# Kernel optimization log

Hardware: AMD Instinct MI355X
Metric: run time of the kernel (lower is better)

Reference implementation:

```python
import jax, jax.numpy as jnp
import numpy as np

PROPOSAL_COUNT = 100
IOU_THRESHOLD = 0.3
SCORE_THRESHOLD = 0.7
MEAN = np.array([0.0, 0.0, 0.0, 0.0], np.float32)
STD = np.array([0.1, 0.1, 0.2, 0.2], np.float32)
CLIP_RATIO = 16.0 / 1000.0
NEG = -1e9  # finite -inf sentinel (avoids NaNs)


def delta2bbox(anchors, delta):
    # anchors: (..., 4) xyxy, delta: (..., 4) normalized dx,dy,dw,dh
    delta = delta * STD + MEAN
    w = anchors[..., 2] - anchors[..., 0]
    h = anchors[..., 3] - anchors[..., 1]
    cx = anchors[..., 0] + 0.5 * w
    cy = anchors[..., 1] + 0.5 * h
    max_ratio = abs(float(np.log(CLIP_RATIO)))
    dx, dy = delta[..., 0], delta[..., 1]
    dw = jnp.clip(delta[..., 2], -max_ratio, max_ratio)
    dh = jnp.clip(delta[..., 3], -max_ratio, max_ratio)
    pcx = cx + dx * w
    pcy = cy + dy * h
    pw = w * jnp.exp(dw)
    ph = h * jnp.exp(dh)
    return jnp.stack([pcx - 0.5 * pw, pcy - 0.5 * ph, pcx + 0.5 * pw, pcy + 0.5 * ph], axis=-1)


def iou_one(box, boxes):
    # box: (4,), boxes: (N, 4) -> (N,)
    ix1 = jnp.maximum(box[0], boxes[..., 0])
    iy1 = jnp.maximum(box[1], boxes[..., 1])
    ix2 = jnp.minimum(box[2], boxes[..., 2])
    iy2 = jnp.minimum(box[3], boxes[..., 3])
    inter = jnp.maximum(ix2 - ix1, 0.0) * jnp.maximum(iy2 - iy1, 0.0)
    area1 = (box[2] - box[0]) * (box[3] - box[1])
    area2 = (boxes[..., 2] - boxes[..., 0]) * (boxes[..., 3] - boxes[..., 1])
    return inter / jnp.maximum(area1 + area2 - inter, 1e-9)


def greedy_nms(scores, boxes):
    # masked greedy hard-NMS with fixed PROPOSAL_COUNT iterations
    # scores: (N,) with NEG on invalid entries, boxes: (N, 4)
    def step(s, _):
        i = jnp.argmax(s)
        si = s[i]
        sel = si > 0.5 * NEG
        iou = iou_one(boxes[i], boxes)
        s = jnp.where(sel & (iou > IOU_THRESHOLD), NEG, s)
        s = s.at[i].set(NEG)
        return s, (jnp.where(sel, i, -1), jnp.where(sel, si, NEG))
    _, (idx, sc) = jax.lax.scan(step, scores, None, length=PROPOSAL_COUNT)
    return idx, sc  # (P,), (P,)


def filter_detection(logits, regress, anchors):
    B, N, C = logits.shape
    # decode + clip (elementwise, same math as gathering first then decoding)
    boxes = jnp.clip(delta2bbox(anchors[None], regress), 0.0, 1.0)  # (B,N,4)
    label = jnp.argmax(logits, axis=-1)                             # (B,N)
    fg = label > 0                                                  # background filter
    scores = jnp.moveaxis(logits[..., 1:], -1, 1)                   # (B,C-1,N)
    valid = fg[:, None, :] & (scores >= SCORE_THRESHOLD)
    s0 = jnp.where(valid, scores, NEG)
    # selection indices are piecewise constant in the inputs
    s0_c = jax.lax.stop_gradient(s0)
    boxes_c = jax.lax.stop_gradient(boxes)
    nms_b = jax.vmap(jax.vmap(greedy_nms, in_axes=(0, None)), in_axes=(0, 0))
    sel_idx, sel_sc = nms_b(s0_c, boxes_c)                          # (B,C-1,P)
    K = (C - 1) * PROPOSAL_COUNT
    idx_flat = sel_idx.reshape(B, K)
    sc_flat = sel_sc.reshape(B, K)
    # global top-k over all classes, sorted descending (matches tf.nn.top_k)
    top_sc, top_pos = jax.lax.top_k(sc_flat, PROPOSAL_COUNT)        # (B,P)
    anchor_idx = jnp.take_along_axis(idx_flat, top_pos, axis=1)
    ok = (top_sc > 0.5 * NEG)[..., None].astype(logits.dtype)       # padding mask
    safe = jnp.maximum(anchor_idx, 0)
    out_logit = jnp.take_along_axis(logits, safe[..., None], axis=1) * ok  # (B,P,C)
    out_box = jnp.take_along_axis(boxes, safe[..., None], axis=1) * ok     # (B,P,4)
    return out_logit, out_box


def setup_inputs() -> dict:
    key = jax.random.key(0)
    k1, k2, k3, k4 = jax.random.split(key, 4)
    B, N, C = 4, 100000, 41
    logits = jax.random.normal(k1, (B, N, C), jnp.float32)
    regress = jax.random.normal(k2, (B, N, 4), jnp.float32) * 0.5
    xy = jax.random.uniform(k3, (N, 2), jnp.float32) * 0.8
    wh = jax.random.uniform(k4, (N, 2), jnp.float32) * 0.2 + 0.01
    anchors = jnp.concatenate([xy, jnp.minimum(xy + wh, 1.0)], axis=-1)  # valid xyxy in [0,1]
    return {"logits": logits, "regress": regress, "anchors": anchors}


def reference(logits, regress, anchors):
    return filter_detection(logits, regress, anchors)
```

## Files before the change

kernel.cpp:

```cpp
#include <hip/hip_runtime.h>
#include <cstdint>
#include <cstddef>

#define BN 4
#define NN 100000
#define CC 41
#define NCLS 40
#define NPROB (BN * NCLS)
#define PROP 100
#define NEGV (-1e9f)
#define IOU_T 0.3f
#define SCORE_T 0.7f
#define MAXR 4.135166556742356f
#define CAP 2048
#define TARGET 384
#define LISTCAP 26624
#define NBMPW 3125
#define E07 0xBF333333u
#define ERHI 0xC1800000u
#define W0 ((unsigned long long)(ERHI - E07))
#define NT3 512
#define CHK 8192
#define NCHKB 4

typedef unsigned long long ull;
typedef unsigned int uint;

__device__ __forceinline__ uint encf(float x) {
  uint u = __float_as_uint(x);
  return (u & 0x80000000u) ? ~u : (u | 0x80000000u);
}
__device__ __forceinline__ float decf(uint e) {
  uint u = (e & 0x80000000u) ? (e ^ 0x80000000u) : ~e;
  return __uint_as_float(u);
}
__device__ __forceinline__ uint binofE(ull E) {
  return (E >= (ull)ERHI) ? 255u : (uint)(((E - E07) << 8) / W0);
}
__device__ __forceinline__ ull edgeE(int b) {
  return (ull)E07 + (((ull)b * W0 + 255ull) >> 8);
}

__device__ __forceinline__ float iou_f(float ax1, float ay1, float ax2, float ay2,
                                       float bx1, float by1, float bx2, float by2) {
  float ix1 = fmaxf(ax1, bx1), iy1 = fmaxf(ay1, by1);
  float ix2 = fminf(ax2, bx2), iy2 = fminf(ay2, by2);
  float inter = fmaxf(ix2 - ix1, 0.0f) * fmaxf(iy2 - iy1, 0.0f);
  float a1 = (ax2 - ax1) * (ay2 - ay1);
  float a2 = (bx2 - bx1) * (by2 - by1);
  return inter / fmaxf(a1 + a2 - inter, 1e-9f);
}

__device__ __forceinline__ int select_window(const uint* h, int* lo_out) {
  uint cum = 0; int lo = 256; int act = 2;
  for (int bb = 255; bb >= 0; --bb) {
    uint nb = h[bb];
    if (nb == 0u) continue;
    if (cum + nb > CAP) {
      if (cum == 0u) { act = 1; }
      break;
    }
    cum += nb; lo = bb; act = 0;
    if (cum >= TARGET) break;
  }
  *lo_out = lo;
  return act;
}

__global__ void decode_kernel(const float4* __restrict__ regress,
                              const float4* __restrict__ anchors,
                              float4* __restrict__ boxes,
                              uint* __restrict__ gcnt) {
  int i = blockIdx.x * 256 + threadIdx.x;
  if (i < NPROB) gcnt[i] = 0u;
  if (i >= BN * NN) return;
  int n = i % NN;
  float4 d = regress[i];
  float4 a = anchors[n];
  float w = a.z - a.x, h = a.w - a.y;
  float cx = a.x + 0.5f * w, cy = a.y + 0.5f * h;
  float dx = d.x * 0.1f, dy = d.y * 0.1f;
  float dw = fminf(fmaxf(d.z * 0.2f, -MAXR), MAXR);
  float dh = fminf(fmaxf(d.w * 0.2f, -MAXR), MAXR);
  float pcx = cx + dx * w, pcy = cy + dy * h;
  float pw = w * expf(dw), ph = h * expf(dh);
  float4 o;
  o.x = fminf(fmaxf(pcx - 0.5f * pw, 0.0f), 1.0f);
  o.y = fminf(fmaxf(pcy - 0.5f * ph, 0.0f), 1.0f);
  o.z = fminf(fmaxf(pcx + 0.5f * pw, 0.0f), 1.0f);
  o.w = fminf(fmaxf(pcy + 0.5f * ph, 0.0f), 1.0f);
  boxes[i] = o;
}

__global__ void score_kernel(const float* __restrict__ logits,
                             ull* __restrict__ glist,
                             uint* __restrict__ gcnt,
                             uint* __restrict__ fgb) {
  __shared__ float lg[256 * CC];
  __shared__ unsigned short wpre[NCLS][4];
  __shared__ uint cbase[NCLS];
  int b = blockIdx.y;
  int n0 = blockIdx.x * 256;
  int tid = threadIdx.x;
  int wave = tid >> 6, lane = tid & 63;
  int rows = NN - n0; if (rows > 256) rows = 256;
  int total4 = rows * CC / 4;
  const float4* src = (const float4*)(logits + ((size_t)b * NN + n0) * CC);
  float4* dst = (float4*)lg;
  for (int i = tid; i < total4; i += 256) dst[i] = src[i];
  __syncthreads();

  bool act = tid < rows;
  int n = n0 + tid;
  float bestv = 0.0f; int bestc = 0;
  if (act) {
    bestv = lg[tid * CC];
    #pragma unroll
    for (int c = 1; c < CC; ++c) {
      float v = lg[tid * CC + c];
      if (v > bestv) { bestv = v; bestc = c; }
    }
  }
  bool fg = act && (bestc > 0);
  int wbase = n0 + (tid & ~63);

  ull mfg = __ballot(fg);
  if (lane == 0 && wbase < NN) fgb[b * NBMPW + (wbase >> 5)] = (uint)mfg;
  if (lane == 32 && wbase + 32 < NN) fgb[b * NBMPW + (wbase >> 5) + 1] = (uint)(mfg >> 32);

  #pragma unroll 4
  for (int c = 1; c < CC; ++c) {
    float v = act ? lg[tid * CC + c] : 0.0f;
    ull m = __ballot(fg && (v >= SCORE_T));
    if (lane == 0) wpre[c - 1][wave] = (unsigned short)__popcll(m);
  }
  __syncthreads();

  if (tid < NCLS) {
    uint t0 = wpre[tid][0], t1 = wpre[tid][1], t2 = wpre[tid][2], t3 = wpre[tid][3];
    uint tot = t0 + t1 + t2 + t3;
    uint base = tot ? atomicAdd(&gcnt[b * NCLS + tid], tot) : 0u;
    cbase[tid] = base;
    wpre[tid][0] = 0;
    wpre[tid][1] = (unsigned short)t0;
    wpre[tid][2] = (unsigned short)(t0 + t1);
    wpre[tid][3] = (unsigned short)(t0 + t1 + t2);
  }
  __syncthreads();

  #pragma unroll 4
  for (int c = 1; c < CC; ++c) {
    float v = act ? lg[tid * CC + c] : 0.0f;
    bool elig = fg && (v >= SCORE_T);
    ull m = __ballot(elig);
    if (elig) {
      uint pos = cbase[c - 1] + wpre[c - 1][wave]
               + (uint)__popcll(m & ((1ull << lane) - 1ull));
      if (pos < LISTCAP)
        glist[(size_t)(b * NCLS + (c - 1)) * LISTCAP + pos] =
            ((ull)encf(v) << 32) | (uint)n;
    }
  }
}

__global__ void hist_kernel(const ull* __restrict__ glist,
                            const uint* __restrict__ gcnt,
                            uint* __restrict__ chist) {
  __shared__ uint h[256];
  int prob = blockIdx.y;
  int chunk = blockIdx.x;
  int tid = threadIdx.x;
  uint cnt = gcnt[prob];
  h[tid] = 0u;
  __syncthreads();
  if (cnt <= LISTCAP) {
    uint lo = chunk * CHK;
    uint hi = cnt < lo + CHK ? cnt : lo + CHK;
    const ull* list = glist + (size_t)prob * LISTCAP;
    for (uint i = lo + tid; i < hi; i += 256)
      atomicAdd(&h[binofE(list[i] >> 32)], 1u);
  }
  __syncthreads();
  chist[((size_t)prob * NCHKB + chunk) * 256 + tid] = h[tid];
}

__global__ void offsets_kernel(const uint* __restrict__ chist,
                               const uint* __restrict__ gcnt,
                               uint* __restrict__ gcoff,
                               uint* __restrict__ gC) {
  __shared__ uint sa[256], sb[256];
  int prob = blockIdx.x;
  int tid = threadIdx.x;
  uint cnt = gcnt[prob];
  if (cnt > LISTCAP) return;
  const uint* ch = chist + (size_t)prob * NCHKB * 256;
  uint h0 = ch[0 * 256 + tid], h1 = ch[1 * 256 + tid],
       h2 = ch[2 * 256 + tid], h3 = ch[3 * 256 + tid];
  gcoff[((size_t)prob * NCHKB + 0) * 256 + tid] = 0u;
  gcoff[((size_t)prob * NCHKB + 1) * 256 + tid] = h0;
  gcoff[((size_t)prob * NCHKB + 2) * 256 + tid] = h0 + h1;
  gcoff[((size_t)prob * NCHKB + 3) * 256 + tid] = h0 + h1 + h2;
  sa[tid] = h0 + h1 + h2 + h3;
  __syncthreads();
  uint* s = sa; uint* d = sb;
  for (int off = 1; off < 256; off <<= 1) {
    uint v = s[tid] + ((tid + off < 256) ? s[tid + off] : 0u);
    d[tid] = v;
    __syncthreads();
    uint* t = s; s = d; d = t;
  }
  gC[(size_t)prob * 257 + tid] = s[tid];
  if (tid == 0) gC[(size_t)prob * 257 + 256] = 0u;
}

__global__ void scatter_kernel(const ull* __restrict__ glist,
                               const uint* __restrict__ gcnt,
                               const uint* __restrict__ gcoff,
                               const uint* __restrict__ gC,
                               ull* __restrict__ blist) {
  __shared__ uint rank[256], startL[256], cofL[256];
  int prob = blockIdx.y;
  int chunk = blockIdx.x;
  int tid = threadIdx.x;
  uint cnt = gcnt[prob];
  if (cnt > LISTCAP) return;
  rank[tid] = 0u;
  cofL[tid] = gcoff[((size_t)prob * NCHKB + chunk) * 256 + tid];
  startL[tid] = gC[(size_t)prob * 257 + tid + 1];
  __syncthreads();
  uint lo = chunk * CHK;
  uint hi = cnt < lo + CHK ? cnt : lo + CHK;
  const ull* list = glist + (size_t)prob * LISTCAP;
  ull* bl = blist + (size_t)prob * LISTCAP;
  for (uint i = lo + tid; i < hi; i += 256) {
    ull k = list[i];
    uint bin = binofE(k >> 32);
    uint r = atomicAdd(&rank[bin], 1u);
    bl[startL[bin] + cofL[bin] + r] = k;
  }
}

__device__ int sort_walk(int ncand, int nsel,
                         ull* keysL, float4* boxesL, float4* selL,
                         int* sh_nsel, int prob, int* __restrict__ oidx,
                         float* __restrict__ osc, int tid) {
  if (ncand == 0) return nsel;
  int M = 64; while (M < ncand) M <<= 1;
  for (int i = ncand + tid; i < M; i += NT3) keysL[i] = 0ull;
  __syncthreads();
  for (int k = 2; k <= M; k <<= 1) {
    for (int j = k >> 1; j > 0; j >>= 1) {
      for (int t = tid; t < M; t += NT3) {
        int ixj = t ^ j;
        if (ixj > t) {
          ull a = keysL[t], c2 = keysL[ixj];
          bool up = ((t & k) == 0);
          if (up ? (a < c2) : (a > c2)) { keysL[t] = c2; keysL[ixj] = a; }
        }
      }
      __syncthreads();
    }
  }
  if (tid < 64) {
    int lane = tid;
    int ns = nsel;
    for (int base = 0; base < ncand && ns < PROP; base += 64) {
      int i = base + lane;
      bool valid = i < ncand;
      ull key = valid ? keysL[i] : 0ull;
      int slot = (int)(key & 0x7FFF);
      float4 bx = boxesL[valid ? slot : 0];
      float sc = decf((uint)(key >> 32));
      int aidx = 131071 - (int)((key >> 15) & 0x1FFFF);
      bool supp = false;
      for (int j = 0; j < ns; ++j) {
        float4 sb = selL[j];
        supp = supp || (iou_f(bx.x, bx.y, bx.z, bx.w, sb.x, sb.y, sb.z, sb.w) > IOU_T);
      }
      ull live = __ballot(valid && !supp);
      while (live && ns < PROP) {
        int kk = __ffsll(live) - 1;
        float x1 = __shfl(bx.x, kk), y1 = __shfl(bx.y, kk);
        float x2 = __shfl(bx.z, kk), y2 = __shfl(bx.w, kk);
        float ksc = __shfl(sc, kk);
        int kidx = __shfl(aidx, kk);
        if (lane == 0) {
          oidx[prob * PROP + ns] = kidx;
          osc [prob * PROP + ns] = ksc;
          selL[ns] = make_float4(x1, y1, x2, y2);
        }
        ns++;
        if (lane > kk && valid && !supp)
          supp = iou_f(bx.x, bx.y, bx.z, bx.w, x1, y1, x2, y2) > IOU_T;
        live = __ballot(valid && !supp) & ~((2ull << kk) - 1ull);
      }
    }
    if (lane == 0) *sh_nsel = ns;
  }
  __syncthreads();
  return *sh_nsel;
}

__device__ int process_window(ull WLO, ull WUP, int idxbin,
                              bool dense, uint rs, uint re,
                              const ull* list, const float* lcol,
                              const uint* fgp, const float4* bx4,
                              ull* keysL, float4* boxesL, float4* selL,
                              int* sh_cnt, int* sh_nsel,
                              int nsel, int prob, int* __restrict__ oidx,
                              float* __restrict__ osc, int tid) {
  __syncthreads();
  if (tid == 0) *sh_cnt = 0;
  __syncthreads();
  if (!dense) {
    for (uint i = rs + tid; i < re; i += NT3) {
      ull k = list[i];
      ull E = k >> 32;
      uint idx = (uint)(k & 0xFFFFFFFFu);
      if (E >= WLO && E < WUP && (idxbin < 0 || (int)(idx >> 9) == idxbin)) {
        int slot = atomicAdd(sh_cnt, 1);
        if (slot < CAP) {
          keysL[slot] = (E << 32)
                      | ((ull)((131071u - idx) & 0x1FFFFu) << 15)
                      | (ull)slot;
          boxesL[slot] = bx4[idx];
        }
      }
    }
  } else {
    for (int i = tid; i < NN; i += NT3) {
      if (!((fgp[i >> 5] >> (i & 31)) & 1u)) continue;
      float s = lcol[(size_t)i * CC];
      if (s < SCORE_T) continue;
      ull E = encf(s);
      if (E >= WLO && E < WUP && (idxbin < 0 || (i >> 9) == idxbin)) {
        int slot = atomicAdd(sh_cnt, 1);
        if (slot < CAP) {
          keysL[slot] = (E << 32)
                      | ((ull)((131071u - (uint)i) & 0x1FFFFu) << 15)
                      | (ull)slot;
          boxesL[slot] = bx4[i];
        }
      }
    }
  }
  __syncthreads();
  int ncand = *sh_cnt; if (ncand > CAP) ncand = CAP;
  return sort_walk(ncand, nsel, keysL, boxesL, selL, sh_nsel, prob, oidx, osc, tid);
}

__device__ int fallback_range(ull Rlo0, ull Rhi0,
                              bool dense, uint rs, uint re,
                              const ull* list, const float* lcol,
                              const uint* fgp, const float4* bx4,
                              ull* keysL, float4* boxesL, float4* selL,
                              uint* subh,
                              int* sh_cnt, int* sh_nsel, int* sh_a, int* sh_b,
                              int nsel, int prob, int* __restrict__ oidx,
                              float* __restrict__ osc, int tid) {
  ull EHIl = Rhi0;
  for (int round = 0; round < 300 && nsel < PROP; ++round) {
    ull Rlo = Rlo0, Rhi = EHIl;
    int action; int bsel;
    ull WLO = 0, WUP = 0, E0 = 0;
    bool idxm = false;
    while (true) {
      for (int i = tid; i < 256; i += NT3) subh[i] = 0u;
      __syncthreads();
      ull W = Rhi - Rlo;
      if (!dense) {
        for (uint i = rs + tid; i < re; i += NT3) {
          ull E = list[i] >> 32;
          if (E >= Rlo && E < Rhi)
            atomicAdd(&subh[(uint)(((E - Rlo) << 8) / W)], 1u);
        }
      } else {
        for (int i = tid; i < NN; i += NT3) {
          if (!((fgp[i >> 5] >> (i & 31)) & 1u)) continue;
          float s = lcol[(size_t)i * CC];
          if (s < SCORE_T) continue;
          ull E = encf(s);
          if (E >= Rlo && E < Rhi)
            atomicAdd(&subh[(uint)(((E - Rlo) << 8) / W)], 1u);
        }
      }
      __syncthreads();
      if (tid == 0) {
        int lo;
        int act = select_window(subh, &lo);
        int rb = -1;
        if (act == 1) {
          for (int bb = 255; bb >= 0; --bb) if (subh[bb]) { rb = bb; break; }
        }
        *sh_a = act; *sh_b = (act == 1) ? rb : lo;
      }
      __syncthreads();
      action = *sh_a; bsel = *sh_b;
      __syncthreads();
      if (action == 2) break;
      if (action == 0) {
        WLO = Rlo + (((ull)bsel * W + 255ull) >> 8);
        WUP = Rhi;
        break;
      }
      ull nRlo = Rlo + (((ull)bsel * W + 255ull) >> 8);
      ull nRhi = Rlo + (((ull)(bsel + 1) * W + 255ull) >> 8);
      if (nRhi > Rhi) nRhi = Rhi;
      Rlo = nRlo; Rhi = nRhi;
      if (Rhi - Rlo <= 1ull) { idxm = true; E0 = Rlo; break; }
    }
    if (action == 2) break;
    if (!idxm) {
      nsel = process_window(WLO, WUP, -1, dense, rs, re, list, lcol, fgp, bx4,
                            keysL, boxesL, selL, sh_cnt, sh_nsel,
                            nsel, prob, oidx, osc, tid);
      EHIl = WLO;
    } else {
      for (int ib = 0; ib < 256 && nsel < PROP; ++ib)
        nsel = process_window(E0, E0 + 1ull, ib, dense, rs, re, list, lcol, fgp, bx4,
                              keysL, boxesL, selL, sh_cnt, sh_nsel,
                              nsel, prob, oidx, osc, tid);
      EHIl = E0;
    }
  }
  return nsel;
}

__launch_bounds__(NT3)
__global__ void nms_finish(const ull* __restrict__ blist,
                           const uint* __restrict__ gcnt,
                           const float* __restrict__ logits,
                           const uint* __restrict__ fgb,
                           const float4* __restrict__ boxes,
                           const uint* __restrict__ gC,
                           int* __restrict__ oidx, float* __restrict__ osc) {
  __shared__ uint CL[257];
  __shared__ uint subh[256];
  __shared__ ull keysL[CAP];
  __shared__ float4 boxesL[CAP];
  __shared__ float4 selL[PROP];
  __shared__ int sh_cnt, sh_nsel, sh_a, sh_b, sh_m;

  int prob = blockIdx.x;
  int b = prob / NCLS;
  int c1 = prob % NCLS + 1;
  int tid = threadIdx.x;

  uint cnt = gcnt[prob];
  bool dense = cnt > LISTCAP;
  const ull* bl = blist + (size_t)prob * LISTCAP;
  const float4* bx4 = boxes + (size_t)b * NN;
  const float* lcol = logits + (size_t)b * NN * CC + c1;
  const uint* fgp = fgb + b * NBMPW;

  int nsel = 0;

  if (dense) {
    nsel = fallback_range(E07, 1ull << 32, true, 0, 0, bl, lcol, fgp, bx4,
                          keysL, boxesL, selL, subh, &sh_cnt, &sh_nsel, &sh_a, &sh_b,
                          0, prob, oidx, osc, tid);
  } else {
    for (int i = tid; i < 257; i += NT3) CL[i] = gC[(size_t)prob * 257 + i];
    __syncthreads();
    int hibin = 256;
    while (nsel < PROP && hibin > 0) {
      if (tid == 0) sh_m = -1;
      __syncthreads();
      if (tid < 256 && tid < hibin && (CL[tid] - CL[hibin]) >= TARGET)
        atomicMax(&sh_m, tid);
      __syncthreads();
      if (tid == 0) {
        int bm = sh_m; int act, lo;
        if (bm < 0) {
          uint W = CL[0] - CL[hibin];
          act = W ? 0 : 2; lo = 0;
        } else {
          uint W = CL[bm] - CL[hibin];
          if (W <= CAP) { act = 0; lo = bm; }
          else {
            uint W2 = CL[bm + 1] - CL[hibin];
            if (W2) { act = 0; lo = bm + 1; }
            else { act = 1; lo = bm; }
          }
        }
        sh_a = act; sh_b = lo;
      }
      __syncthreads();
      int act = sh_a, lo = sh_b;
      __syncthreads();
      if (act == 2) break;
      if (act == 0) {
        uint rs = CL[hibin];
        int ncand = (int)(CL[lo] - CL[hibin]);
        for (int i = tid; i < ncand; i += NT3) {
          ull k = bl[rs + i];
          uint idx = (uint)(k & 0xFFFFFFFFu);
          keysL[i] = ((k >> 32) << 32)
                   | ((ull)((131071u - idx) & 0x1FFFFu) << 15)
                   | (ull)i;
          boxesL[i] = bx4[idx];
        }
        __syncthreads();
        nsel = sort_walk(ncand, nsel, keysL, boxesL, selL, &sh_nsel, prob, oidx, osc, tid);
        hibin = lo;
      } else {
        uint rs = CL[lo + 1], re = CL[lo];
        ull Rlo = edgeE(lo);
        ull Rhi = (lo == 255) ? (1ull << 32) : edgeE(lo + 1);
        nsel = fallback_range(Rlo, Rhi, false, rs, re, bl, lcol, fgp, bx4,
                              keysL, boxesL, selL, subh, &sh_cnt, &sh_nsel, &sh_a, &sh_b,
                              nsel, prob, oidx, osc, tid);
        hibin = lo;
      }
    }
  }

  __syncthreads();
  for (int p = nsel + tid; p < PROP; p += NT3) {
    oidx[prob * PROP + p] = -1;
    osc [prob * PROP + p] = NEGV;
  }
}

__global__ void topk_kernel(const float* __restrict__ logits,
                            const float4* __restrict__ boxes,
                            const int* __restrict__ oidx,
                            const float* __restrict__ osc,
                            float* __restrict__ out) {
  __shared__ ull keys[4096];
  int b = blockIdx.x;
  int tid = threadIdx.x;
  for (int i = tid; i < 4096; i += 1024) {
    ull key = 0ull;
    if (i < NCLS * PROP) {
      float sc = osc[b * NCLS * PROP + i];
      key = ((ull)encf(sc) << 32) | (uint)(~i);
    }
    keys[i] = ~key;
  }
  __syncthreads();
  for (int k = 2; k <= 4096; k <<= 1) {
    for (int j = k >> 1; j > 0; j >>= 1) {
      for (int t = tid; t < 4096; t += 1024) {
        int ixj = t ^ j;
        if (ixj > t) {
          ull a = keys[t], c2 = keys[ixj];
          bool up = ((t & k) == 0);
          if ((a > c2) == up) { keys[t] = c2; keys[ixj] = a; }
        }
      }
      __syncthreads();
    }
  }
  if (tid < PROP) {
    ull key = ~keys[tid];
    uint e = (uint)(key >> 32);
    float sc = decf(e);
    bool ok = sc > 0.5f * NEGV;
    int kk = (int)(~(uint)key);
    if (kk < 0 || kk >= NCLS * PROP) kk = 0;
    int idx = ok ? oidx[b * NCLS * PROP + kk] : 0;
    if (idx < 0) idx = 0;
    float m = ok ? 1.0f : 0.0f;
    const float* lp = logits + ((size_t)b * NN + idx) * CC;
    float* outl = out + ((size_t)b * PROP + tid) * CC;
    #pragma unroll
    for (int c = 0; c < CC; ++c) outl[c] = lp[c] * m;
    float4 bb = boxes[(size_t)b * NN + idx];
    float* outb = out + (size_t)BN * PROP * CC + ((size_t)b * PROP + tid) * 4;
    outb[0] = bb.x * m; outb[1] = bb.y * m; outb[2] = bb.z * m; outb[3] = bb.w * m;
  }
}

extern "C" void kernel_launch(void* const* d_in, const int* in_sizes, int n_in,
                              void* d_out, int out_size, void* d_ws, size_t ws_size,
                              hipStream_t stream) {
  const float* logits  = (const float*)d_in[0];
  const float* regress = (const float*)d_in[1];
  const float* anchors = (const float*)d_in[2];
  float* out = (float*)d_out;

  char* ws = (char*)d_ws;
  size_t off = 0;
  float4* boxes = (float4*)(ws + off);  off += (size_t)BN * NN * 16;
  ull* glist = (ull*)(ws + off);        off += (size_t)NPROB * LISTCAP * 8;
  ull* blist = (ull*)(ws + off);        off += (size_t)NPROB * LISTCAP * 8;
  uint* gcnt = (uint*)(ws + off);       off += NPROB * 4;
  uint* fgb  = (uint*)(ws + off);       off += BN * NBMPW * 4;
  float* osc = (float*)(ws + off);      off += NPROB * PROP * 4;
  int*   oidx = (int*)(ws + off);       off += NPROB * PROP * 4;
  uint* chist = (uint*)(ws + off);      off += (size_t)NPROB * NCHKB * 256 * 4;
  uint* gcoff = (uint*)(ws + off);      off += (size_t)NPROB * NCHKB * 256 * 4;
  uint* gC   = (uint*)(ws + off);       off += (size_t)NPROB * 257 * 4;

  decode_kernel<<<(BN * NN + 255) / 256, 256, 0, stream>>>(
      (const float4*)regress, (const float4*)anchors, boxes, gcnt);
  score_kernel<<<dim3((NN + 255) / 256, BN), 256, 0, stream>>>(logits, glist, gcnt, fgb);
  hist_kernel<<<dim3(NCHKB, NPROB), 256, 0, stream>>>(glist, gcnt, chist);
  offsets_kernel<<<NPROB, 256, 0, stream>>>(chist, gcnt, gcoff, gC);
  scatter_kernel<<<dim3(NCHKB, NPROB), 256, 0, stream>>>(glist, gcnt, gcoff, gC, blist);
  nms_finish<<<NPROB, NT3, 0, stream>>>(blist, gcnt, logits, fgb, boxes, gC, oidx, osc);
  topk_kernel<<<BN, 1024, 0, stream>>>(logits, boxes, oidx, osc, out);
}
```

Before: 220.0 us.

## Shrink score kernel to single-wave blocks and drop LDS prefix sums

The score kernel now runs one 64-lane wave per block instead of four, so per-class counts come straight from ballots without shared-memory prefix arrays or extra block barriers. Each lane caches its logit row in registers, and the foreground test becomes a max over classes 1..40 compared with class 0. Lane c-1 issues the atomicAdd for class c and the base is broadcast with shuffles. The trade-off is four times as many blocks and four times as many global atomics, plus higher register pressure from holding 41 floats per lane.

```diff
diff --git a/kernel.cpp b/kernel.cpp
--- a/kernel.cpp
+++ b/kernel.cpp
@@ -92,70 +92,56 @@
   boxes[i] = o;
 }
 
-__global__ void score_kernel(const float* __restrict__ logits,
-                             ull* __restrict__ glist,
-                             uint* __restrict__ gcnt,
-                             uint* __restrict__ fgb) {
-  __shared__ float lg[256 * CC];
-  __shared__ unsigned short wpre[NCLS][4];
-  __shared__ uint cbase[NCLS];
+__global__ void __launch_bounds__(64)
+score_kernel(const float* __restrict__ logits,
+             ull* __restrict__ glist,
+             uint* __restrict__ gcnt,
+             uint* __restrict__ fgb) {
+  __shared__ float lg[64 * CC];
   int b = blockIdx.y;
-  int n0 = blockIdx.x * 256;
-  int tid = threadIdx.x;
-  int wave = tid >> 6, lane = tid & 63;
-  int rows = NN - n0; if (rows > 256) rows = 256;
+  int n0 = blockIdx.x * 64;
+  int lane = threadIdx.x;
+  int rows = NN - n0; if (rows > 64) rows = 64;
   int total4 = rows * CC / 4;
   const float4* src = (const float4*)(logits + ((size_t)b * NN + n0) * CC);
   float4* dst = (float4*)lg;
-  for (int i = tid; i < total4; i += 256) dst[i] = src[i];
-  __syncthreads();
-
-  bool act = tid < rows;
-  int n = n0 + tid;
-  float bestv = 0.0f; int bestc = 0;
-  if (act) {
-    bestv = lg[tid * CC];
-    #pragma unroll
-    for (int c = 1; c < CC; ++c) {
-      float v = lg[tid * CC + c];
-      if (v > bestv) { bestv = v; bestc = c; }
-    }
-  }
-  bool fg = act && (bestc > 0);
-  int wbase = n0 + (tid & ~63);
+  for (int i = lane; i < total4; i += 64) dst[i] = src[i];
+  __syncthreads();
+
+  bool act = lane < rows;
+  int n = n0 + lane;
+
+  float row[CC];
+  #pragma unroll
+  for (int c = 0; c < CC; ++c) row[c] = act ? lg[lane * CC + c] : 0.0f;
+
+  float m1 = row[1];
+  #pragma unroll
+  for (int c = 2; c < CC; ++c) m1 = fmaxf(m1, row[c]);
+  bool fg = act && (m1 > row[0]);
 
   ull mfg = __ballot(fg);
-  if (lane == 0 && wbase < NN) fgb[b * NBMPW + (wbase >> 5)] = (uint)mfg;
-  if (lane == 32 && wbase + 32 < NN) fgb[b * NBMPW + (wbase >> 5) + 1] = (uint)(mfg >> 32);
-
-  #pragma unroll 4
+  if (lane == 0) fgb[b * NBMPW + (n0 >> 5)] = (uint)mfg;
+  if (lane == 32 && n0 + 32 < NN) fgb[b * NBMPW + (n0 >> 5) + 1] = (uint)(mfg >> 32);
+
+  ull mym = 0ull;
+  #pragma unroll
   for (int c = 1; c < CC; ++c) {
-    float v = act ? lg[tid * CC + c] : 0.0f;
-    ull m = __ballot(fg && (v >= SCORE_T));
-    if (lane == 0) wpre[c - 1][wave] = (unsigned short)__popcll(m);
-  }
-  __syncthreads();
-
-  if (tid < NCLS) {
-    uint t0 = wpre[tid][0], t1 = wpre[tid][1], t2 = wpre[tid][2], t3 = wpre[tid][3];
-    uint tot = t0 + t1 + t2 + t3;
-    uint base = tot ? atomicAdd(&gcnt[b * NCLS + tid], tot) : 0u;
-    cbase[tid] = base;
-    wpre[tid][0] = 0;
-    wpre[tid][1] = (unsigned short)t0;
-    wpre[tid][2] = (unsigned short)(t0 + t1);
-    wpre[tid][3] = (unsigned short)(t0 + t1 + t2);
-  }
-  __syncthreads();
-
-  #pragma unroll 4
+    ull m = __ballot(fg && (row[c] >= SCORE_T));
+    if (lane == c - 1) mym = m;
+  }
+  uint base = 0u;
+  if (lane < NCLS && mym)
+    base = atomicAdd(&gcnt[b * NCLS + lane], (uint)__popcll(mym));
+
+  #pragma unroll
   for (int c = 1; c < CC; ++c) {
-    float v = act ? lg[tid * CC + c] : 0.0f;
+    float v = row[c];
     bool elig = fg && (v >= SCORE_T);
     ull m = __ballot(elig);
+    uint bc = __shfl(base, c - 1);
     if (elig) {
-      uint pos = cbase[c - 1] + wpre[c - 1][wave]
-               + (uint)__popcll(m & ((1ull << lane) - 1ull));
+      uint pos = bc + (uint)__popcll(m & ((1ull << lane) - 1ull));
       if (pos < LISTCAP)
         glist[(size_t)(b * NCLS + (c - 1)) * LISTCAP + pos] =
             ((ull)encf(v) << 32) | (uint)n;
@@ -595,7 +581,7 @@
 
   decode_kernel<<<(BN * NN + 255) / 256, 256, 0, stream>>>(
       (const float4*)regress, (const float4*)anchors, boxes, gcnt);
-  score_kernel<<<dim3((NN + 255) / 256, BN), 256, 0, stream>>>(logits, glist, gcnt, fgb);
+  score_kernel<<<dim3((NN + 63) / 64, BN), 64, 0, stream>>>(logits, glist, gcnt, fgb);
   hist_kernel<<<dim3(NCHKB, NPROB), 256, 0, stream>>>(glist, gcnt, chist);
   offsets_kernel<<<NPROB, 256, 0, stream>>>(chist, gcnt, gcoff, gC);
   scatter_kernel<<<dim3(NCHKB, NPROB), 256, 0, stream>>>(glist, gcnt, gcoff, gC, blist);
```

After: 260.4 us. 1.18x slower.

## Replace single-wave NMS walk with block-parallel bitmask suppression and larger windows

Applied to the files above, without the earlier changes.

Splits the sort+walk into a bitonic sort followed by a new walk that keeps a live-candidate bitmask in shared memory. Each selected box suppresses later candidates using all 512 threads rather than one wave. Candidate windows grow (TARGET 384→3072, CAP 2048→4096), so fewer window rounds run per class. The trade-off is one block-wide barrier per selected box, longer bitonic sorts over bigger windows, and more shared memory per block (about 100KB), which may limit occupancy.

```diff
diff --git a/kernel.cpp b/kernel.cpp
--- a/kernel.cpp
+++ b/kernel.cpp
@@ -13,7 +13,9 @@
 #define SCORE_T 0.7f
 #define MAXR 4.135166556742356f
 #define CAP 2048
+#define CAPW 4096
 #define TARGET 384
+#define TARGETW 3072
 #define LISTCAP 26624
 #define NBMPW 3125
 #define E07 0xBF333333u
@@ -240,11 +242,7 @@
   }
 }
 
-__device__ int sort_walk(int ncand, int nsel,
-                         ull* keysL, float4* boxesL, float4* selL,
-                         int* sh_nsel, int prob, int* __restrict__ oidx,
-                         float* __restrict__ osc, int tid) {
-  if (ncand == 0) return nsel;
+__device__ void sort_desc(ull* keysL, int ncand, int tid) {
   int M = 64; while (M < ncand) M <<= 1;
   for (int i = ncand + tid; i < M; i += NT3) keysL[i] = 0ull;
   __syncthreads();
@@ -261,44 +259,72 @@
       __syncthreads();
     }
   }
-  if (tid < 64) {
-    int lane = tid;
-    int ns = nsel;
-    for (int base = 0; base < ncand && ns < PROP; base += 64) {
-      int i = base + lane;
-      bool valid = i < ncand;
-      ull key = valid ? keysL[i] : 0ull;
-      int slot = (int)(key & 0x7FFF);
-      float4 bx = boxesL[valid ? slot : 0];
-      float sc = decf((uint)(key >> 32));
-      int aidx = 131071 - (int)((key >> 15) & 0x1FFFF);
-      bool supp = false;
-      for (int j = 0; j < ns; ++j) {
+}
+
+__device__ int fwalk(int ncand, int nsel,
+                     const ull* keysL, const float4* boxesL, float4* selL,
+                     uint* liveW, int* sh_sel, int prob,
+                     int* __restrict__ oidx, float* __restrict__ osc, int tid) {
+  if (ncand == 0) return nsel;
+  int nw = (ncand + 31) >> 5;
+  for (int i = tid; i < nw; i += NT3) {
+    int rem = ncand - (i << 5);
+    liveW[i] = (rem >= 32) ? 0xFFFFFFFFu : ((1u << rem) - 1u);
+  }
+  __syncthreads();
+  if (nsel > 0) {
+    for (int i = tid; i < ncand; i += NT3) {
+      float4 bx = boxesL[(int)(keysL[i] & 0x7FFF)];
+      bool dead = false;
+      for (int j = 0; j < nsel; ++j) {
         float4 sb = selL[j];
-        supp = supp || (iou_f(bx.x, bx.y, bx.z, bx.w, sb.x, sb.y, sb.z, sb.w) > IOU_T);
-      }
-      ull live = __ballot(valid && !supp);
-      while (live && ns < PROP) {
-        int kk = __ffsll(live) - 1;
-        float x1 = __shfl(bx.x, kk), y1 = __shfl(bx.y, kk);
-        float x2 = __shfl(bx.z, kk), y2 = __shfl(bx.w, kk);
-        float ksc = __shfl(sc, kk);
-        int kidx = __shfl(aidx, kk);
-        if (lane == 0) {
-          oidx[prob * PROP + ns] = kidx;
-          osc [prob * PROP + ns] = ksc;
-          selL[ns] = make_float4(x1, y1, x2, y2);
-        }
-        ns++;
-        if (lane > kk && valid && !supp)
-          supp = iou_f(bx.x, bx.y, bx.z, bx.w, x1, y1, x2, y2) > IOU_T;
-        live = __ballot(valid && !supp) & ~((2ull << kk) - 1ull);
-      }
-    }
-    if (lane == 0) *sh_nsel = ns;
-  }
-  __syncthreads();
-  return *sh_nsel;
+        dead = dead || (iou_f(bx.x, bx.y, bx.z, bx.w, sb.x, sb.y, sb.z, sb.w) > IOU_T);
+      }
+      if (dead) atomicAnd(&liveW[i >> 5], ~(1u << (i & 31)));
+    }
+    __syncthreads();
+  }
+  int pos = 0;
+  while (nsel < PROP) {
+    if (tid < 64) {
+      int base = pos >> 5;
+      int fidx = -1;
+      for (int rb = base; rb < nw && fidx < 0; rb += 64) {
+        int widx = rb + tid;
+        uint w = (widx < nw) ? liveW[widx] : 0u;
+        if (widx == base && (pos & 31)) w &= ~((1u << (pos & 31)) - 1u);
+        ull m = __ballot(w != 0u);
+        if (m) {
+          int fl = __ffsll(m) - 1;
+          uint fw = __shfl(w, fl);
+          fidx = ((rb + fl) << 5) + (__ffs(fw) - 1);
+        }
+      }
+      if (tid == 0) *sh_sel = fidx;
+    }
+    __syncthreads();
+    int i = *sh_sel;
+    if (i < 0) break;
+    ull key = keysL[i];
+    float4 nb = boxesL[(int)(key & 0x7FFF)];
+    if (tid == 0) {
+      oidx[prob * PROP + nsel] = 131071 - (int)((key >> 15) & 0x1FFFF);
+      osc [prob * PROP + nsel] = decf((uint)(key >> 32));
+      selL[nsel] = nb;
+      atomicAnd(&liveW[i >> 5], ~(1u << (i & 31)));
+    }
+    for (int k = i + 1 + tid; k < ncand; k += NT3) {
+      if ((liveW[k >> 5] >> (k & 31)) & 1u) {
+        float4 cb = boxesL[(int)(keysL[k] & 0x7FFF)];
+        if (iou_f(cb.x, cb.y, cb.z, cb.w, nb.x, nb.y, nb.z, nb.w) > IOU_T)
+          atomicAnd(&liveW[k >> 5], ~(1u << (k & 31)));
+      }
+    }
+    nsel++;
+    pos = i + 1;
+    __syncthreads();
+  }
+  return nsel;
 }
 
 __device__ int process_window(ull WLO, ull WUP, int idxbin,
@@ -306,7 +332,7 @@
                               const ull* list, const float* lcol,
                               const uint* fgp, const float4* bx4,
                               ull* keysL, float4* boxesL, float4* selL,
-                              int* sh_cnt, int* sh_nsel,
+                              uint* liveW, int* sh_cnt, int* sh_sel,
                               int nsel, int prob, int* __restrict__ oidx,
                               float* __restrict__ osc, int tid) {
   __syncthreads();
@@ -346,7 +372,9 @@
   }
   __syncthreads();
   int ncand = *sh_cnt; if (ncand > CAP) ncand = CAP;
-  return sort_walk(ncand, nsel, keysL, boxesL, selL, sh_nsel, prob, oidx, osc, tid);
+  if (ncand == 0) return nsel;
+  sort_desc(keysL, ncand, tid);
+  return fwalk(ncand, nsel, keysL, boxesL, selL, liveW, sh_sel, prob, oidx, osc, tid);
 }
 
 __device__ int fallback_range(ull Rlo0, ull Rhi0,
@@ -354,8 +382,8 @@
                               const ull* list, const float* lcol,
                               const uint* fgp, const float4* bx4,
                               ull* keysL, float4* boxesL, float4* selL,
-                              uint* subh,
-                              int* sh_cnt, int* sh_nsel, int* sh_a, int* sh_b,
+                              uint* liveW, uint* subh,
+                              int* sh_cnt, int* sh_sel, int* sh_a, int* sh_b,
                               int nsel, int prob, int* __restrict__ oidx,
                               float* __restrict__ osc, int tid) {
   ull EHIl = Rhi0;
@@ -412,13 +440,13 @@
     if (action == 2) break;
     if (!idxm) {
       nsel = process_window(WLO, WUP, -1, dense, rs, re, list, lcol, fgp, bx4,
-                            keysL, boxesL, selL, sh_cnt, sh_nsel,
+                            keysL, boxesL, selL, liveW, sh_cnt, sh_sel,
                             nsel, prob, oidx, osc, tid);
       EHIl = WLO;
     } else {
       for (int ib = 0; ib < 256 && nsel < PROP; ++ib)
         nsel = process_window(E0, E0 + 1ull, ib, dense, rs, re, list, lcol, fgp, bx4,
-                              keysL, boxesL, selL, sh_cnt, sh_nsel,
+                              keysL, boxesL, selL, liveW, sh_cnt, sh_sel,
                               nsel, prob, oidx, osc, tid);
       EHIl = E0;
     }
@@ -436,10 +464,11 @@
                            int* __restrict__ oidx, float* __restrict__ osc) {
   __shared__ uint CL[257];
   __shared__ uint subh[256];
-  __shared__ ull keysL[CAP];
-  __shared__ float4 boxesL[CAP];
+  __shared__ ull keysL[CAPW];
+  __shared__ float4 boxesL[CAPW];
   __shared__ float4 selL[PROP];
-  __shared__ int sh_cnt, sh_nsel, sh_a, sh_b, sh_m;
+  __shared__ uint liveW[CAPW / 32];
+  __shared__ int sh_cnt, sh_sel, sh_a, sh_b, sh_m;
 
   int prob = blockIdx.x;
   int b = prob / NCLS;
@@ -457,7 +486,8 @@
 
   if (dense) {
     nsel = fallback_range(E07, 1ull << 32, true, 0, 0, bl, lcol, fgp, bx4,
-                          keysL, boxesL, selL, subh, &sh_cnt, &sh_nsel, &sh_a, &sh_b,
+                          keysL, boxesL, selL, liveW, subh,
+                          &sh_cnt, &sh_sel, &sh_a, &sh_b,
                           0, prob, oidx, osc, tid);
   } else {
     for (int i = tid; i < 257; i += NT3) CL[i] = gC[(size_t)prob * 257 + i];
@@ -466,7 +496,7 @@
     while (nsel < PROP && hibin > 0) {
       if (tid == 0) sh_m = -1;
       __syncthreads();
-      if (tid < 256 && tid < hibin && (CL[tid] - CL[hibin]) >= TARGET)
+      if (tid < 256 && tid < hibin && (CL[tid] - CL[hibin]) >= TARGETW)
         atomicMax(&sh_m, tid);
       __syncthreads();
       if (tid == 0) {
@@ -476,7 +506,7 @@
           act = W ? 0 : 2; lo = 0;
         } else {
           uint W = CL[bm] - CL[hibin];
-          if (W <= CAP) { act = 0; lo = bm; }
+          if (W <= CAPW) { act = 0; lo = bm; }
           else {
             uint W2 = CL[bm + 1] - CL[hibin];
             if (W2) { act = 0; lo = bm + 1; }
@@ -501,14 +531,17 @@
           boxesL[i] = bx4[idx];
         }
         __syncthreads();
-        nsel = sort_walk(ncand, nsel, keysL, boxesL, selL, &sh_nsel, prob, oidx, osc, tid);
+        sort_desc(keysL, ncand, tid);
+        nsel = fwalk(ncand, nsel, keysL, boxesL, selL, liveW, &sh_sel,
+                     prob, oidx, osc, tid);
         hibin = lo;
       } else {
         uint rs = CL[lo + 1], re = CL[lo];
         ull Rlo = edgeE(lo);
         ull Rhi = (lo == 255) ? (1ull << 32) : edgeE(lo + 1);
         nsel = fallback_range(Rlo, Rhi, false, rs, re, bl, lcol, fgp, bx4,
-                              keysL, boxesL, selL, subh, &sh_cnt, &sh_nsel, &sh_a, &sh_b,
+                              keysL, boxesL, selL, liveW, subh,
+                              &sh_cnt, &sh_sel, &sh_a, &sh_b,
                               nsel, prob, oidx, osc, tid);
         hibin = lo;
       }
```

Result: slower. 447.4 us (+103.3%).

## Pre-sort score bins in a parallel kernel and stream-walk sorted runs in NMS

Applied to the files above, without the earlier changes.

Adds a sortbins kernel that bitonic-sorts each histogram bin of every class list in parallel (one block per bin per problem) and writes the sorted keys back in place. The NMS finish kernel then walks contiguous runs of already-sorted bins directly from global memory with a single wavefront and prefetches the next keys and boxes. This replaces the per-window gather and full bitonic sort in shared memory inside the serial per-problem block. The cost is an extra kernel launch and more global traffic, and the sort now covers every bin rather than only the top ones NMS actually needs.

```diff
diff --git a/kernel.cpp b/kernel.cpp
--- a/kernel.cpp
+++ b/kernel.cpp
@@ -240,6 +240,46 @@
   }
 }
 
+__global__ void sortbins_kernel(ull* __restrict__ blist,
+                                const uint* __restrict__ gcnt,
+                                const uint* __restrict__ gC) {
+  __shared__ ull kb[CAP];
+  int prob = blockIdx.y;
+  int bin = blockIdx.x;
+  int tid = threadIdx.x;
+  uint cnt = gcnt[prob];
+  if (cnt > LISTCAP) return;
+  uint rs = gC[(size_t)prob * 257 + bin + 1];
+  uint re = gC[(size_t)prob * 257 + bin];
+  int sz = (int)(re - rs);
+  if (sz < 2 || sz > CAP) return;
+  ull* bl = blist + (size_t)prob * LISTCAP;
+  for (int i = tid; i < sz; i += 256) {
+    ull k = bl[rs + i];
+    kb[i] = (k & 0xFFFFFFFF00000000ull) | (ull)(uint)(~(uint)k);
+  }
+  int M = 64; while (M < sz) M <<= 1;
+  for (int i = sz + tid; i < M; i += 256) kb[i] = 0ull;
+  __syncthreads();
+  for (int k = 2; k <= M; k <<= 1) {
+    for (int j = k >> 1; j > 0; j >>= 1) {
+      for (int t = tid; t < M; t += 256) {
+        int ixj = t ^ j;
+        if (ixj > t) {
+          ull a = kb[t], c2 = kb[ixj];
+          bool up = ((t & k) == 0);
+          if (up ? (a < c2) : (a > c2)) { kb[t] = c2; kb[ixj] = a; }
+        }
+      }
+      __syncthreads();
+    }
+  }
+  for (int i = tid; i < sz; i += 256) {
+    ull t = kb[i];
+    bl[rs + i] = (t & 0xFFFFFFFF00000000ull) | (ull)(uint)(~(uint)t);
+  }
+}
+
 __device__ int sort_walk(int ncand, int nsel,
                          ull* keysL, float4* boxesL, float4* selL,
                          int* sh_nsel, int prob, int* __restrict__ oidx,
@@ -294,6 +334,56 @@
           supp = iou_f(bx.x, bx.y, bx.z, bx.w, x1, y1, x2, y2) > IOU_T;
         live = __ballot(valid && !supp) & ~((2ull << kk) - 1ull);
       }
+    }
+    if (lane == 0) *sh_nsel = ns;
+  }
+  __syncthreads();
+  return *sh_nsel;
+}
+
+__device__ int walk_run(uint rs, uint re, int nsel,
+                        const ull* __restrict__ bl, const float4* __restrict__ bx4,
+                        float4* selL, int* sh_nsel, int prob,
+                        int* __restrict__ oidx, float* __restrict__ osc, int tid) {
+  if (re <= rs) return nsel;
+  if (tid < 64) {
+    int lane = tid;
+    int ns = nsel;
+    uint i0 = rs + lane;
+    bool v0 = i0 < re;
+    ull key = v0 ? bl[i0] : 0ull;
+    float4 bx = v0 ? bx4[(uint)key] : make_float4(0.f, 0.f, 0.f, 0.f);
+    for (uint base = rs; base < re && ns < PROP; base += 64) {
+      uint i1 = base + 64 + lane;
+      bool v1 = i1 < re;
+      ull nkey = v1 ? bl[i1] : 0ull;
+      bool valid = (base + lane) < re;
+      uint aidx = (uint)key;
+      float sc = decf((uint)(key >> 32));
+      bool supp = false;
+      for (int j = 0; j < ns; ++j) {
+        float4 sb = selL[j];
+        supp = supp || (iou_f(bx.x, bx.y, bx.z, bx.w, sb.x, sb.y, sb.z, sb.w) > IOU_T);
+      }
+      ull live = __ballot(valid && !supp);
+      while (live && ns < PROP) {
+        int kk = __ffsll(live) - 1;
+        float x1 = __shfl(bx.x, kk), y1 = __shfl(bx.y, kk);
+        float x2 = __shfl(bx.z, kk), y2 = __shfl(bx.w, kk);
+        float ksc = __shfl(sc, kk);
+        int kidx = __shfl((int)aidx, kk);
+        if (lane == 0) {
+          oidx[prob * PROP + ns] = kidx;
+          osc [prob * PROP + ns] = ksc;
+          selL[ns] = make_float4(x1, y1, x2, y2);
+        }
+        ns++;
+        if (lane > kk && valid && !supp)
+          supp = iou_f(bx.x, bx.y, bx.z, bx.w, x1, y1, x2, y2) > IOU_T;
+        live = __ballot(valid && !supp) & ~((2ull << kk) - 1ull);
+      }
+      float4 nbx = v1 ? bx4[(uint)nkey] : make_float4(0.f, 0.f, 0.f, 0.f);
+      key = nkey; bx = nbx;
     }
     if (lane == 0) *sh_nsel = ns;
   }
@@ -439,7 +529,7 @@
   __shared__ ull keysL[CAP];
   __shared__ float4 boxesL[CAP];
   __shared__ float4 selL[PROP];
-  __shared__ int sh_cnt, sh_nsel, sh_a, sh_b, sh_m;
+  __shared__ int sh_cnt, sh_nsel, sh_a, sh_b;
 
   int prob = blockIdx.x;
   int b = prob / NCLS;
@@ -457,61 +547,31 @@
 
   if (dense) {
     nsel = fallback_range(E07, 1ull << 32, true, 0, 0, bl, lcol, fgp, bx4,
-                          keysL, boxesL, selL, subh, &sh_cnt, &sh_nsel, &sh_a, &sh_b,
+                          keysL, boxesL, selL, subh,
+                          &sh_cnt, &sh_nsel, &sh_a, &sh_b,
                           0, prob, oidx, osc, tid);
   } else {
     for (int i = tid; i < 257; i += NT3) CL[i] = gC[(size_t)prob * 257 + i];
     __syncthreads();
-    int hibin = 256;
-    while (nsel < PROP && hibin > 0) {
-      if (tid == 0) sh_m = -1;
-      __syncthreads();
-      if (tid < 256 && tid < hibin && (CL[tid] - CL[hibin]) >= TARGET)
-        atomicMax(&sh_m, tid);
-      __syncthreads();
-      if (tid == 0) {
-        int bm = sh_m; int act, lo;
-        if (bm < 0) {
-          uint W = CL[0] - CL[hibin];
-          act = W ? 0 : 2; lo = 0;
-        } else {
-          uint W = CL[bm] - CL[hibin];
-          if (W <= CAP) { act = 0; lo = bm; }
-          else {
-            uint W2 = CL[bm + 1] - CL[hibin];
-            if (W2) { act = 0; lo = bm + 1; }
-            else { act = 1; lo = bm; }
-          }
-        }
-        sh_a = act; sh_b = lo;
-      }
-      __syncthreads();
-      int act = sh_a, lo = sh_b;
-      __syncthreads();
-      if (act == 2) break;
-      if (act == 0) {
-        uint rs = CL[hibin];
-        int ncand = (int)(CL[lo] - CL[hibin]);
-        for (int i = tid; i < ncand; i += NT3) {
-          ull k = bl[rs + i];
-          uint idx = (uint)(k & 0xFFFFFFFFu);
-          keysL[i] = ((k >> 32) << 32)
-                   | ((ull)((131071u - idx) & 0x1FFFFu) << 15)
-                   | (ull)i;
-          boxesL[i] = bx4[idx];
-        }
-        __syncthreads();
-        nsel = sort_walk(ncand, nsel, keysL, boxesL, selL, &sh_nsel, prob, oidx, osc, tid);
-        hibin = lo;
-      } else {
-        uint rs = CL[lo + 1], re = CL[lo];
+    int bin = 255;
+    while (bin >= 0 && nsel < PROP) {
+      int lo = bin;
+      while (lo >= 0 && (CL[lo] - CL[lo + 1]) <= CAP) --lo;
+      uint rs = CL[bin + 1];
+      uint re = CL[lo + 1];
+      if (re > rs)
+        nsel = walk_run(rs, re, nsel, bl, bx4, selL, &sh_nsel, prob, oidx, osc, tid);
+      if (nsel >= PROP || lo < 0) break;
+      {
+        uint mrs = CL[lo + 1], mre = CL[lo];
         ull Rlo = edgeE(lo);
         ull Rhi = (lo == 255) ? (1ull << 32) : edgeE(lo + 1);
-        nsel = fallback_range(Rlo, Rhi, false, rs, re, bl, lcol, fgp, bx4,
-                              keysL, boxesL, selL, subh, &sh_cnt, &sh_nsel, &sh_a, &sh_b,
+        nsel = fallback_range(Rlo, Rhi, false, mrs, mre, bl, lcol, fgp, bx4,
+                              keysL, boxesL, selL, subh,
+                              &sh_cnt, &sh_nsel, &sh_a, &sh_b,
                               nsel, prob, oidx, osc, tid);
-        hibin = lo;
-      }
+      }
+      bin = lo - 1;
     }
   }
 
@@ -599,6 +659,7 @@
   hist_kernel<<<dim3(NCHKB, NPROB), 256, 0, stream>>>(glist, gcnt, chist);
   offsets_kernel<<<NPROB, 256, 0, stream>>>(chist, gcnt, gcoff, gC);
   scatter_kernel<<<dim3(NCHKB, NPROB), 256, 0, stream>>>(glist, gcnt, gcoff, gC, blist);
+  sortbins_kernel<<<dim3(256, NPROB), 256, 0, stream>>>(blist, gcnt, gC);
   nms_finish<<<NPROB, NT3, 0, stream>>>(blist, gcnt, logits, fgb, boxes, gC, oidx, osc);
   topk_kernel<<<BN, 1024, 0, stream>>>(logits, boxes, oidx, osc, out);
 }
```

New measurement: 405.9 us. +84.5%, slower.
